# Performance work log

Measured on AMD Instinct MI355X. Metric: run time of the kernel, lower is better.

## Reference

```python
import jax, jax.numpy as jnp
import numpy as np

N_KW, N_RT = 100000, 20000
D, H, O = 128, 128, 128
E_A, E_B, E_C = 1600000, 1600000, 320000


def setup_inputs() -> dict:
    key = jax.random.key(0)
    ks = jax.random.split(key, 32)
    inp = {
        "x_kw": jax.random.normal(ks[0], (N_KW, D), jnp.float32),
        "x_rt": jax.random.normal(ks[1], (N_RT, D), jnp.float32),
        "src_a": jax.random.randint(ks[2], (E_A,), 0, N_RT),
        "dst_a": jax.random.randint(ks[3], (E_A,), 0, N_KW),
        "src_b": jax.random.randint(ks[4], (E_B,), 0, N_KW),
        "dst_b": jax.random.randint(ks[5], (E_B,), 0, N_KW),
        "src_c": jax.random.randint(ks[6], (E_C,), 0, N_RT),
        "dst_c": jax.random.randint(ks[7], (E_C,), 0, N_RT),
    }
    # SAGEConv params per relation per layer: W_l (neighbor), b_l, W_r (root, no bias)
    i = 8
    dims = {1: (D, H), 2: (H, O)}
    for layer in (1, 2):
        din, dout = dims[layer]
        for rel in ("a", "b", "c"):
            inp[f"Wl{layer}{rel}"] = jax.random.normal(ks[i], (din, dout), jnp.float32) * 0.05; i += 1
            inp[f"bl{layer}{rel}"] = jnp.zeros((dout,), jnp.float32)
            inp[f"Wr{layer}{rel}"] = jax.random.normal(ks[i], (din, dout), jnp.float32) * 0.05; i += 1
    return inp


def _sage(x_src, x_dst, src, dst, Wl, bl, Wr):
    # PyG SAGEConv (mean aggr): lin_l(mean_j x_src[j]) + lin_r(x_dst)
    n = x_dst.shape[0]
    s = jax.ops.segment_sum(x_src[src], dst, num_segments=n)      # [n, din]
    cnt = jax.ops.segment_sum(jnp.ones_like(dst, dtype=x_src.dtype), dst, num_segments=n)
    mean = s / jnp.maximum(cnt, 1.0)[:, None]
    return mean @ Wl + bl + x_dst @ Wr


def reference(x_kw, x_rt, src_a, dst_a, src_b, dst_b, src_c, dst_c,
              Wl1a, bl1a, Wr1a, Wl1b, bl1b, Wr1b, Wl1c, bl1c, Wr1c,
              Wl2a, bl2a, Wr2a, Wl2b, bl2b, Wr2b, Wl2c, bl2c, Wr2c):
    # layer 1 (HeteroConv aggr='sum' over relations sharing a dst type)
    kw1 = (_sage(x_rt, x_kw, src_a, dst_a, Wl1a, bl1a, Wr1a)
           + _sage(x_kw, x_kw, src_b, dst_b, Wl1b, bl1b, Wr1b))
    rt1 = _sage(x_rt, x_rt, src_c, dst_c, Wl1c, bl1c, Wr1c)
    kw1 = jax.nn.relu(kw1)
    rt1 = jax.nn.relu(rt1)
    # layer 2
    kw2 = (_sage(rt1, kw1, src_a, dst_a, Wl2a, bl2a, Wr2a)
           + _sage(kw1, kw1, src_b, dst_b, Wl2b, bl2b, Wr2b))
    rt2 = _sage(rt1, rt1, src_c, dst_c, Wl2c, bl2c, Wr2c)
    return kw2, rt2
```

## Files before the change

kernel.cpp:

```cpp
#include <hip/hip_runtime.h>

typedef __attribute__((ext_vector_type(8))) short bf16x8;
typedef __attribute__((ext_vector_type(4))) float f32x4;
typedef __attribute__((ext_vector_type(2))) float f32x2;

static __device__ __forceinline__ unsigned short f2bf(float f) {
    unsigned int u = __float_as_uint(f);
    u += 0x7fffu + ((u >> 16) & 1u);
    return (unsigned short)(u >> 16);
}
static __device__ __forceinline__ float bf2f(unsigned short h) {
    return __uint_as_float(((unsigned int)h) << 16);
}

#define BSH 6
#define BUCKET 64
#define NBMAX 1600
#define CHSH 13


struct PrepArgs {
    const float* W[10];
    const float* Wa[10];
    const float* b1a; const float* b1b; const float* b2a; const float* b2b;
};

__global__ void prep_k(PrepArgs pa, unsigned short* __restrict__ Wt,
                       float* __restrict__ bc1, float* __restrict__ bc2) {
    int blk = blockIdx.x;
    if (blk < 640) {
        int slot = blk >> 6;
        int i = ((blk & 63) << 8) + threadIdx.x;
        float v = pa.W[slot][i];
        const float* w2 = pa.Wa[slot];
        if (w2) v += w2[i];
        int k = i >> 7, n = i & 127;
        Wt[slot * 16384 + n * 128 + k] = f2bf(v);
    } else {
        int t = threadIdx.x;
        if (t < 128) bc1[t] = pa.b1a[t] + pa.b1b[t];
        else bc2[t - 128] = pa.b2a[t - 128] + pa.b2b[t - 128];
    }
}


struct Rel {
    const int* src; const int* dst; int E; int nb; int Ndst;
    int hblk0, hnblk;
    int sblk0, snblk;
    int oblk0;
    int* bcnt; int* boff; int* bcur;
    unsigned* pairs; unsigned* ssrc; int* goff; float* invd;
};
struct Rels { Rel r[3]; };

__global__ void bhist3_k(Rels R) {
    const Rel* r;
    int bid = blockIdx.x;
    if (bid < R.r[1].hblk0) r = &R.r[0];
    else if (bid < R.r[2].hblk0) r = &R.r[1];
    else r = &R.r[2];
    __shared__ int h[NBMAX];
    for (int i = threadIdx.x; i < r->nb; i += 256) h[i] = 0;
    __syncthreads();
    for (int e = (bid - r->hblk0) * 256 + threadIdx.x; e < r->E; e += r->hnblk * 256)
        atomicAdd(&h[r->dst[e] >> BSH], 1);
    __syncthreads();
    for (int i = threadIdx.x; i < r->nb; i += 256)
        if (h[i]) atomicAdd(&r->bcnt[i], h[i]);
}

__global__ void bscan3_k(Rels R) {
    const Rel* r = &R.r[blockIdx.x];
    __shared__ int s[1024];
    int t = threadIdx.x;
    int nb = r->nb;
    int e0 = 2 * t, e1 = 2 * t + 1;
    int v0 = (e0 < nb) ? r->bcnt[e0] : 0;
    int v1 = (e1 < nb) ? r->bcnt[e1] : 0;
    s[t] = v0 + v1;
    __syncthreads();
    for (int o = 1; o < 1024; o <<= 1) {
        int x = (t >= o) ? s[t - o] : 0;
        __syncthreads();
        s[t] += x;
        __syncthreads();
    }
    int P = s[t] - (v0 + v1);
    if (e0 <= nb) { r->boff[e0] = P; if (e0 < nb) r->bcur[e0] = 0; }
    if (e1 <= nb) { r->boff[e1] = P + v0; if (e1 < nb) r->bcur[e1] = 0; }
}

__global__ __launch_bounds__(256) void bscatter3_k(Rels R) {
    const Rel* r;
    int bid = blockIdx.x;
    if (bid < R.r[1].sblk0) r = &R.r[0];
    else if (bid < R.r[2].sblk0) r = &R.r[1];
    else r = &R.r[2];
    __shared__ int h[NBMAX];
    __shared__ int base[NBMAX];
    int t = threadIdx.x;
    int nb = r->nb, E = r->E;
    for (int i = t; i < nb; i += 256) h[i] = 0;
    __syncthreads();
    int e0 = (bid - r->sblk0) * 8192;
    for (int i = 0; i < 32; i++) {
        int e = e0 + i * 256 + t;
        if (e < E) atomicAdd(&h[r->dst[e] >> BSH], 1);
    }
    __syncthreads();
    for (int i = t; i < nb; i += 256) {
        int c = h[i];
        base[i] = c ? (r->boff[i] + atomicAdd(&r->bcur[i], c)) : 0;
    }
    __syncthreads();
    for (int i = t; i < nb; i += 256) h[i] = 0;
    __syncthreads();
    for (int i = 0; i < 32; i++) {
        int e = e0 + i * 256 + t;
        if (e < E) {
            int d = r->dst[e];
            int b = d >> BSH;
            int pos = base[b] + atomicAdd(&h[b], 1);
            r->pairs[pos] = ((unsigned)(d & (BUCKET - 1)) << 17) | (unsigned)r->src[e];
        }
    }
}

__global__ __launch_bounds__(256) void sortb3_k(Rels R) {
    const Rel* r;
    int bid = blockIdx.x;
    if (bid < R.r[1].oblk0) r = &R.r[0];
    else if (bid < R.r[2].oblk0) r = &R.r[1];
    else r = &R.r[2];
    int b = bid - r->oblk0;
    __shared__ int cnt[1024];
    __shared__ int sc[256];
    int t = threadIdx.x;
    for (int i = t; i < 1024; i += 256) cnt[i] = 0;
    __syncthreads();
    int j0 = r->boff[b], j1 = r->boff[b + 1];
    for (int j = j0 + t; j < j1; j += 256) {
        unsigned p = r->pairs[j];
        int d = (p >> 17) & 63;
        int ch = (int)((p & 0x1ffffu) >> CHSH); if (ch > 15) ch = 15;
        int bin = ((d & 7) << 7) | ((d >> 3) << 4) | ch;
        atomicAdd(&cnt[bin], 1);
    }
    __syncthreads();
    if (t < 64) {
        int b0 = ((t & 7) << 7) | ((t >> 3) << 4);
        int c = 0;
#pragma unroll
        for (int i = 0; i < 16; i++) c += cnt[b0 + i];
        int dd = (b << BSH) + t;
        if (dd < r->Ndst) r->invd[dd] = 1.f / (float)(c > 0 ? c : 1);
    }
    int c0 = cnt[4 * t], c1 = cnt[4 * t + 1], c2 = cnt[4 * t + 2], c3 = cnt[4 * t + 3];
    int tot = c0 + c1 + c2 + c3;
    sc[t] = tot;
    __syncthreads();
    for (int o = 1; o < 256; o <<= 1) {
        int x = (t >= o) ? sc[t - o] : 0;
        __syncthreads();
        sc[t] += x;
        __syncthreads();
    }
    int base = j0 + sc[t] - tot;
    if ((t & 3) == 0) r->goff[b * 64 + (t >> 2)] = base;
    cnt[4 * t] = base;
    cnt[4 * t + 1] = base + c0;
    cnt[4 * t + 2] = base + c0 + c1;
    cnt[4 * t + 3] = base + c0 + c1 + c2;
    if (t == 0 && b == r->nb - 1) r->goff[r->nb * 64] = r->E;
    __syncthreads();
    for (int j = j0 + t; j < j1; j += 256) {
        unsigned p = r->pairs[j];
        int d = (p >> 17) & 63;
        int ch = (int)((p & 0x1ffffu) >> CHSH); if (ch > 15) ch = 15;
        int bin = ((d & 7) << 7) | ((d >> 3) << 4) | ch;
        int pos = atomicAdd(&cnt[bin], 1);
        r->ssrc[pos] = p & 0x1ffffu;
    }
}


struct GemmJobs {
    const void* Akw; int Nkw;
    const unsigned short* Wk1; const float* bk; unsigned short* Zkw;
    const unsigned short* Wk2; unsigned short* Ckw;
    const void* Art; int Nrt;
    const unsigned short* Wr1; const float* br; unsigned short* Zrt;
    const unsigned short* Wr2; unsigned short* Crt2;
    const unsigned short* Wr3; unsigned short* Crt3;
    int kwBlocks;
};

template <int AF32>
__global__ __launch_bounds__(256) void gemm3_k(GemmJobs G) {
    int bid = blockIdx.x;
    bool iskw = bid < G.kwBlocks;
    const void* A = iskw ? G.Akw : G.Art;
    int N = iskw ? G.Nkw : G.Nrt;
    int lane = threadIdx.x & 63;
    int r16 = lane & 15, g = lane >> 4;
    int row0 = (iskw ? bid : bid - G.kwBlocks) * 64 + (threadIdx.x >> 6) * 16;
    int arow = row0 + r16;
    int arow_c = arow < N ? arow : N - 1;

    bf16x8 af[4];
    if (AF32) {
        const float* Af = (const float*)A + (size_t)arow_c * 128 + g * 8;
#pragma unroll
        for (int kc = 0; kc < 4; kc++) {
            float4 u0 = *(const float4*)(Af + kc * 32);
            float4 u1 = *(const float4*)(Af + kc * 32 + 4);
            bf16x8 r;
            r[0] = (short)f2bf(u0.x); r[1] = (short)f2bf(u0.y);
            r[2] = (short)f2bf(u0.z); r[3] = (short)f2bf(u0.w);
            r[4] = (short)f2bf(u1.x); r[5] = (short)f2bf(u1.y);
            r[6] = (short)f2bf(u1.z); r[7] = (short)f2bf(u1.w);
            af[kc] = r;
        }
    } else {
        const bf16x8* Ar = (const bf16x8*)((const unsigned short*)A + (size_t)arow_c * 128);
#pragma unroll
        for (int kc = 0; kc < 4; kc++) af[kc] = Ar[kc * 4 + g];
    }

    if (iskw) {
        f32x4 acc1[8], acc2[8];
#pragma unroll
        for (int ct = 0; ct < 8; ct++) { f32x4 z = {0.f,0.f,0.f,0.f}; acc1[ct] = z; acc2[ct] = z; }
#pragma unroll
        for (int kc = 0; kc < 4; kc++) {
#pragma unroll
            for (int ct = 0; ct < 8; ct++) {
                int wo = ((ct * 16 + r16) << 7) + kc * 32 + g * 8;
                bf16x8 b1 = *(const bf16x8*)(G.Wk1 + wo);
                acc1[ct] = __builtin_amdgcn_mfma_f32_16x16x32_bf16(af[kc], b1, acc1[ct], 0, 0, 0);
                bf16x8 b2 = *(const bf16x8*)(G.Wk2 + wo);
                acc2[ct] = __builtin_amdgcn_mfma_f32_16x16x32_bf16(af[kc], b2, acc2[ct], 0, 0, 0);
            }
        }
#pragma unroll
        for (int ct = 0; ct < 8; ct++) {
            int col = ct * 16 + r16;
            float bb = G.bk[col];
#pragma unroll
            for (int j = 0; j < 4; j++) {
                int r = row0 + g * 4 + j;
                if (r < N) {
                    G.Zkw[(size_t)r * 128 + col] = f2bf(acc1[ct][j] + bb);
                    G.Ckw[(size_t)r * 128 + col] = f2bf(acc2[ct][j]);
                }
            }
        }
    } else {
        f32x4 acc1[8], acc2[8], acc3[8];
#pragma unroll
        for (int ct = 0; ct < 8; ct++) {
            f32x4 z = {0.f,0.f,0.f,0.f}; acc1[ct] = z; acc2[ct] = z; acc3[ct] = z;
        }
#pragma unroll
        for (int kc = 0; kc < 4; kc++) {
#pragma unroll
            for (int ct = 0; ct < 8; ct++) {
                int wo = ((ct * 16 + r16) << 7) + kc * 32 + g * 8;
                bf16x8 b1 = *(const bf16x8*)(G.Wr1 + wo);
                acc1[ct] = __builtin_amdgcn_mfma_f32_16x16x32_bf16(af[kc], b1, acc1[ct], 0, 0, 0);
                bf16x8 b2 = *(const bf16x8*)(G.Wr2 + wo);
                acc2[ct] = __builtin_amdgcn_mfma_f32_16x16x32_bf16(af[kc], b2, acc2[ct], 0, 0, 0);
                bf16x8 b3 = *(const bf16x8*)(G.Wr3 + wo);
                acc3[ct] = __builtin_amdgcn_mfma_f32_16x16x32_bf16(af[kc], b3, acc3[ct], 0, 0, 0);
            }
        }
#pragma unroll
        for (int ct = 0; ct < 8; ct++) {
            int col = ct * 16 + r16;
            float bb = G.br[col];
#pragma unroll
            for (int j = 0; j < 4; j++) {
                int r = row0 + g * 4 + j;
                if (r < N) {
                    G.Zrt[(size_t)r * 128 + col] = f2bf(acc1[ct][j] + bb);
                    G.Crt2[(size_t)r * 128 + col] = f2bf(acc2[ct][j]);
                    G.Crt3[(size_t)r * 128 + col] = f2bf(acc3[ct][j]);
                }
            }
        }
    }
}

struct AggJob {
    const unsigned short* Zin; int Ndst;
    const unsigned* sp0; const int* goff0; const float* invd0; const unsigned short* Y0;
    const unsigned* sp1; const int* goff1; const float* invd1; const unsigned short* Y1;
    int nrel;
    float* OutF; unsigned short* OutB;
};

template <int RELU, int OUTBF16>
__global__ __launch_bounds__(512) void bagg2_k(AggJob JK, AggJob JR, int kwBlocks) {
    __shared__ float acc[BUCKET * 128];
    bool iskw = blockIdx.x < kwBlocks;
    AggJob J = iskw ? JK : JR;
    int b = iskw ? blockIdx.x : blockIdx.x - kwBlocks;
    int t = threadIdx.x;
    int dst0 = b << BSH;
    int nrow = J.Ndst - dst0; if (nrow > BUCKET) nrow = BUCKET;

    for (int c = t; c < BUCKET * 32; c += 512) {
        int r = c >> 5, m = c & 31;
        float z0 = 0.f, z1 = 0.f, z2 = 0.f, z3 = 0.f;
        if (r < nrow) {
            ushort4 z = *(const ushort4*)(J.Zin + (size_t)(dst0 + r) * 128 + (m << 2));
            z0 = bf2f(z.x); z1 = bf2f(z.y); z2 = bf2f(z.z); z3 = bf2f(z.w);
        }
        acc[r * 128 + m] = z0;
        acc[r * 128 + 32 + m] = z1;
        acc[r * 128 + 64 + m] = z2;
        acc[r * 128 + 96 + m] = z3;
    }
    __syncthreads();

    int w = t >> 6, lane = t & 63;
    int h = lane >> 5, q = lane & 31;
#pragma unroll 1
    for (int rel = 0; rel < J.nrel; rel++) {
        const unsigned* sp = rel ? J.sp1 : J.sp0;
        const int* goff = rel ? J.goff1 : J.goff0;
        const float* invd = rel ? J.invd1 : J.invd0;
        const unsigned short* Y = rel ? J.Y1 : J.Y0;
#pragma unroll 1
        for (int r = 0; r < 8; r++) {
            int g = b * 64 + w * 8 + r;
            int jg0 = goff[g], jg1 = goff[g + 1];
            if (jg0 >= jg1) continue;
            int d = (r << 3) | w;
            f32x2 a01 = {0.f, 0.f}, a23 = {0.f, 0.f};
#pragma unroll 1
            for (int j = jg0; j < jg1; j += 16) {
                uint2 v[8];
#pragma unroll
                for (int k = 0; k < 8; k++) {
                    int e = j + 2 * k + h;
                    e = e < jg1 ? e : jg1 - 1;
                    int s = (int)sp[e];
                    v[k] = *(const uint2*)(Y + ((size_t)s << 7) + (q << 2));
                }
#pragma unroll
                for (int k = 0; k < 8; k++) {
                    bool ok = (j + 2 * k + h) < jg1;
                    unsigned vx = ok ? v[k].x : 0u;
                    unsigned vy = ok ? v[k].y : 0u;
                    f32x2 x01 = { __uint_as_float(vx << 16),
                                  __uint_as_float(vx & 0xffff0000u) };
                    f32x2 x23 = { __uint_as_float(vy << 16),
                                  __uint_as_float(vy & 0xffff0000u) };
                    a01 += x01;
                    a23 += x23;
                }
            }
            a01.x += __shfl_xor(a01.x, 32); a01.y += __shfl_xor(a01.y, 32);
            a23.x += __shfl_xor(a23.x, 32); a23.y += __shfl_xor(a23.y, 32);
            float inv = invd[dst0 + d];
            float v0 = (h ? a23.x : a01.x) * inv;
            float v1 = (h ? a23.y : a01.y) * inv;
            int ba = d * 128 + q + h * 64;
            acc[ba] += v0;
            acc[ba + 32] += v1;
        }
    }
    __syncthreads();
    for (int c = t; c < BUCKET * 32; c += 512) {
        int r = c >> 5, m = c & 31;
        if (r < nrow) {
            float x0 = acc[r * 128 + m];
            float x1 = acc[r * 128 + 32 + m];
            float x2 = acc[r * 128 + 64 + m];
            float x3 = acc[r * 128 + 96 + m];
            if (RELU) {
                x0 = fmaxf(x0, 0.f); x1 = fmaxf(x1, 0.f);
                x2 = fmaxf(x2, 0.f); x3 = fmaxf(x3, 0.f);
            }
            size_t o = (size_t)(dst0 + r) * 128 + (m << 2);
            if (OUTBF16) {
                ushort4 ov;
                ov.x = f2bf(x0); ov.y = f2bf(x1); ov.z = f2bf(x2); ov.w = f2bf(x3);
                *(ushort4*)(J.OutB + o) = ov;
            } else {
                *(float4*)(J.OutF + o) = make_float4(x0, x1, x2, x3);
            }
        }
    }
}


static inline size_t align256(size_t x) { return (x + 255) & ~size_t(255); }

extern "C" void kernel_launch(void* const* d_in, const int* in_sizes, int n_in,
                              void* d_out, int out_size, void* d_ws, size_t ws_size,
                              hipStream_t stream) {
    const float* x_kw = (const float*)d_in[0];
    const float* x_rt = (const float*)d_in[1];
    const int* src_a = (const int*)d_in[2];
    const int* dst_a = (const int*)d_in[3];
    const int* src_b = (const int*)d_in[4];
    const int* dst_b = (const int*)d_in[5];
    const int* src_c = (const int*)d_in[6];
    const int* dst_c = (const int*)d_in[7];
    const float *Wl1a = (const float*)d_in[8],  *bl1a = (const float*)d_in[9],  *Wr1a = (const float*)d_in[10];
    const float *Wl1b = (const float*)d_in[11], *bl1b = (const float*)d_in[12], *Wr1b = (const float*)d_in[13];
    const float *Wl1c = (const float*)d_in[14], *bl1c = (const float*)d_in[15], *Wr1c = (const float*)d_in[16];
    const float *Wl2a = (const float*)d_in[17], *bl2a = (const float*)d_in[18], *Wr2a = (const float*)d_in[19];
    const float *Wl2b = (const float*)d_in[20], *bl2b = (const float*)d_in[21], *Wr2b = (const float*)d_in[22];
    const float *Wl2c = (const float*)d_in[23], *bl2c = (const float*)d_in[24], *Wr2c = (const float*)d_in[25];

    const int NKW = in_sizes[0] / 128;
    const int NRT = in_sizes[1] / 128;
    const int EA = in_sizes[2], EB = in_sizes[4], EC = in_sizes[6];
    const int nb_kw = (NKW + BUCKET - 1) / BUCKET;
    const int nb_rt = (NRT + BUCKET - 1) / BUCKET;

    char* ws = (char*)d_ws;
    size_t off = 0;
    auto alloc = [&](size_t bytes) -> char* {
        off = align256(off);
        char* p = ws + off;
        off += bytes;
        return p;
    };
    unsigned short* Wt = (unsigned short*)alloc(10 * 16384 * 2);
    float* bc1 = (float*)alloc(128 * 4);
    float* bc2 = (float*)alloc(128 * 4);
    int* bcnt3 = (int*)alloc(3 * NBMAX * 4);
    int* bcur3 = (int*)alloc(3 * NBMAX * 4);
    int* boff_a = (int*)alloc((NBMAX + 1) * 4);
    int* boff_b = (int*)alloc((NBMAX + 1) * 4);
    int* boff_c = (int*)alloc((NBMAX + 1) * 4);
    int* goff_a = (int*)alloc(((size_t)nb_kw * 64 + 1) * 4);
    int* goff_b = (int*)alloc(((size_t)nb_kw * 64 + 1) * 4);
    int* goff_c = (int*)alloc(((size_t)nb_rt * 64 + 1) * 4);
    float* invd_a = (float*)alloc((size_t)NKW * 4);
    float* invd_b = (float*)alloc((size_t)NKW * 4);
    float* invd_c = (float*)alloc((size_t)NRT * 4);
    unsigned* pairs_a = (unsigned*)alloc((size_t)EA * 4);
    unsigned* pairs_b = (unsigned*)alloc((size_t)EB * 4);
    unsigned* pairs_c = (unsigned*)alloc((size_t)EC * 4);
    unsigned* sp_a = (unsigned*)alloc((size_t)EA * 4);
    unsigned* sp_b = (unsigned*)alloc((size_t)EB * 4);
    unsigned* sp_c = (unsigned*)alloc((size_t)EC * 4);
    unsigned short* Yb = (unsigned short*)alloc((size_t)NKW * 128 * 2);
    unsigned short* Zkw = (unsigned short*)alloc((size_t)NKW * 128 * 2);
    unsigned short* Zrt = (unsigned short*)alloc((size_t)NRT * 128 * 2);
    unsigned short* kw1_bf = (unsigned short*)alloc((size_t)NKW * 128 * 2);
    unsigned short* rt1_bf = (unsigned short*)alloc((size_t)NRT * 128 * 2);
    (void)ws_size;
    unsigned short* Ya = (unsigned short*)pairs_b;
    unsigned short* Yc = (unsigned short*)pairs_a;

    float* out_kw = (float*)d_out;
    float* out_rt = out_kw + (size_t)NKW * 128;

    PrepArgs pa;
    pa.W[0] = Wr1a; pa.Wa[0] = Wr1b;
    pa.W[1] = Wl1a; pa.Wa[1] = nullptr;
    pa.W[2] = Wl1b; pa.Wa[2] = nullptr;
    pa.W[3] = Wl1c; pa.Wa[3] = nullptr;
    pa.W[4] = Wr1c; pa.Wa[4] = nullptr;
    pa.W[5] = Wr2a; pa.Wa[5] = Wr2b;
    pa.W[6] = Wl2a; pa.Wa[6] = nullptr;
    pa.W[7] = Wl2b; pa.Wa[7] = nullptr;
    pa.W[8] = Wl2c; pa.Wa[8] = nullptr;
    pa.W[9] = Wr2c; pa.Wa[9] = nullptr;
    pa.b1a = bl1a; pa.b1b = bl1b; pa.b2a = bl2a; pa.b2b = bl2b;
    prep_k<<<641, 256, 0, stream>>>(pa, Wt, bc1, bc2);
    unsigned short* W0 = Wt + 0 * 16384;
    unsigned short* W1 = Wt + 1 * 16384;
    unsigned short* W2 = Wt + 2 * 16384;
    unsigned short* W3 = Wt + 3 * 16384;
    unsigned short* W4 = Wt + 4 * 16384;
    unsigned short* W5 = Wt + 5 * 16384;
    unsigned short* W6 = Wt + 6 * 16384;
    unsigned short* W7 = Wt + 7 * 16384;
    unsigned short* W8 = Wt + 8 * 16384;
    unsigned short* W9 = Wt + 9 * 16384;

    hipMemsetAsync(bcnt3, 0, 3 * NBMAX * 4, stream);
    Rels R;
    int hA = 128, hB = 128, hC = 64;
    int sA = (EA + 8191) / 8192, sB = (EB + 8191) / 8192, sC = (EC + 8191) / 8192;
    R.r[0] = {src_a, dst_a, EA, nb_kw, NKW, 0, hA, 0, sA, 0,
              bcnt3, boff_a, bcur3, pairs_a, sp_a, goff_a, invd_a};
    R.r[1] = {src_b, dst_b, EB, nb_kw, NKW, hA, hB, sA, sB, nb_kw,
              bcnt3 + NBMAX, boff_b, bcur3 + NBMAX, pairs_b, sp_b, goff_b, invd_b};
    R.r[2] = {src_c, dst_c, EC, nb_rt, NRT, hA + hB, hC, sA + sB, sC, 2 * nb_kw,
              bcnt3 + 2 * NBMAX, boff_c, bcur3 + 2 * NBMAX, pairs_c, sp_c, goff_c, invd_c};
    bhist3_k<<<hA + hB + hC, 256, 0, stream>>>(R);
    bscan3_k<<<3, 1024, 0, stream>>>(R);
    bscatter3_k<<<sA + sB + sC, 256, 0, stream>>>(R);
    sortb3_k<<<2 * nb_kw + nb_rt, 256, 0, stream>>>(R);

    const int kwB = (NKW + 63) / 64, rtB = (NRT + 63) / 64;

    GemmJobs G1;
    G1.Akw = x_kw; G1.Nkw = NKW; G1.Wk1 = W0; G1.bk = bc1; G1.Zkw = Zkw; G1.Wk2 = W2; G1.Ckw = Yb;
    G1.Art = x_rt; G1.Nrt = NRT; G1.Wr1 = W4; G1.br = bl1c; G1.Zrt = Zrt;
    G1.Wr2 = W1; G1.Crt2 = Ya; G1.Wr3 = W3; G1.Crt3 = Yc;
    G1.kwBlocks = kwB;
    gemm3_k<1><<<kwB + rtB, 256, 0, stream>>>(G1);

    AggJob JK1 = {Zkw, NKW, sp_a, goff_a, invd_a, Ya, sp_b, goff_b, invd_b, Yb, 2,
                  nullptr, kw1_bf};
    AggJob JR1 = {Zrt, NRT, sp_c, goff_c, invd_c, Yc, nullptr, nullptr, nullptr, nullptr, 1,
                  nullptr, rt1_bf};
    bagg2_k<1, 1><<<nb_kw + nb_rt, 512, 0, stream>>>(JK1, JR1, nb_kw);

    GemmJobs G2;
    G2.Akw = kw1_bf; G2.Nkw = NKW; G2.Wk1 = W5; G2.bk = bc2; G2.Zkw = Zkw; G2.Wk2 = W7; G2.Ckw = Yb;
    G2.Art = rt1_bf; G2.Nrt = NRT; G2.Wr1 = W9; G2.br = bl2c; G2.Zrt = Zrt;
    G2.Wr2 = W6; G2.Crt2 = Ya; G2.Wr3 = W8; G2.Crt3 = Yc;
    G2.kwBlocks = kwB;
    gemm3_k<0><<<kwB + rtB, 256, 0, stream>>>(G2);

    AggJob JK2 = {Zkw, NKW, sp_a, goff_a, invd_a, Ya, sp_b, goff_b, invd_b, Yb, 2,
                  out_kw, nullptr};
    AggJob JR2 = {Zrt, NRT, sp_c, goff_c, invd_c, Yc, nullptr, nullptr, nullptr, nullptr, 1,
                  out_rt, nullptr};
    bagg2_k<0, 0><<<nb_kw + nb_rt, 512, 0, stream>>>(JK2, JR2, nb_kw);
}
```

Before: 580.3 us.

## Store relation-b messages in FP8, pre-shift gather offsets, fuse prep/hist and gemm/sort kernels

The relation-b projected features (kw->kw, the largest edge set) are now written as FP8 instead of BF16, which halves the bytes gathered per edge in aggregation. Sorted source indices are pre-shifted into byte offsets so the gather loop does no index arithmetic. The weight prep kernel is merged with the histogram kernel, and the sort kernel with the layer-1 GEMM, to cut launches and let independent work overlap. The aggregation loop is split into a full-chunk path and a masked tail. The cost is lower precision for one relation's messages, with added accuracy risk, plus separate Ya/Yc buffers instead of reusing the pairs buffers.

New measurement: 595.8 us. 1.03x slower.

```diff
diff --git a/kernel.cpp b/kernel.cpp
--- a/kernel.cpp
+++ b/kernel.cpp
@@ -18,6 +18,17 @@
 #define NBMAX 1600
 #define CHSH 13
 
+
+struct Rel {
+    const int* src; const int* dst; int E; int nb; int Ndst;
+    int hblk0, hnblk;
+    int sblk0, snblk;
+    int oblk0;
+    int shift;
+    int* bcnt; int* boff; int* bcur;
+    unsigned* pairs; unsigned* ssrc; int* goff; float* invd;
+};
+struct Rels { Rel r[3]; };
 
 struct PrepArgs {
     const float* W[10];
@@ -25,50 +36,42 @@
     const float* b1a; const float* b1b; const float* b2a; const float* b2b;
 };
 
-__global__ void prep_k(PrepArgs pa, unsigned short* __restrict__ Wt,
-                       float* __restrict__ bc1, float* __restrict__ bc2) {
-    int blk = blockIdx.x;
-    if (blk < 640) {
-        int slot = blk >> 6;
-        int i = ((blk & 63) << 8) + threadIdx.x;
-        float v = pa.W[slot][i];
-        const float* w2 = pa.Wa[slot];
-        if (w2) v += w2[i];
-        int k = i >> 7, n = i & 127;
-        Wt[slot * 16384 + n * 128 + k] = f2bf(v);
-    } else {
-        int t = threadIdx.x;
-        if (t < 128) bc1[t] = pa.b1a[t] + pa.b1b[t];
-        else bc2[t - 128] = pa.b2a[t - 128] + pa.b2b[t - 128];
-    }
-}
-
-
-struct Rel {
-    const int* src; const int* dst; int E; int nb; int Ndst;
-    int hblk0, hnblk;
-    int sblk0, snblk;
-    int oblk0;
-    int* bcnt; int* boff; int* bcur;
-    unsigned* pairs; unsigned* ssrc; int* goff; float* invd;
-};
-struct Rels { Rel r[3]; };
-
-__global__ void bhist3_k(Rels R) {
+
+__global__ void prep_hist_k(PrepArgs pa, unsigned short* __restrict__ Wt,
+                            float* __restrict__ bc1, float* __restrict__ bc2,
+                            Rels R, int prepBlocks) {
+    int bid = blockIdx.x;
+    if (bid < prepBlocks) {
+        if (bid < 640) {
+            int slot = bid >> 6;
+            int i = ((bid & 63) << 8) + threadIdx.x;
+            float v = pa.W[slot][i];
+            const float* w2 = pa.Wa[slot];
+            if (w2) v += w2[i];
+            int k = i >> 7, n = i & 127;
+            Wt[slot * 16384 + n * 128 + k] = f2bf(v);
+        } else {
+            int t = threadIdx.x;
+            if (t < 128) bc1[t] = pa.b1a[t] + pa.b1b[t];
+            else bc2[t - 128] = pa.b2a[t - 128] + pa.b2b[t - 128];
+        }
+        return;
+    }
+    int hb = bid - prepBlocks;
     const Rel* r;
-    int bid = blockIdx.x;
-    if (bid < R.r[1].hblk0) r = &R.r[0];
-    else if (bid < R.r[2].hblk0) r = &R.r[1];
+    if (hb < R.r[1].hblk0) r = &R.r[0];
+    else if (hb < R.r[2].hblk0) r = &R.r[1];
     else r = &R.r[2];
     __shared__ int h[NBMAX];
     for (int i = threadIdx.x; i < r->nb; i += 256) h[i] = 0;
     __syncthreads();
-    for (int e = (bid - r->hblk0) * 256 + threadIdx.x; e < r->E; e += r->hnblk * 256)
+    for (int e = (hb - r->hblk0) * 256 + threadIdx.x; e < r->E; e += r->hnblk * 256)
         atomicAdd(&h[r->dst[e] >> BSH], 1);
     __syncthreads();
     for (int i = threadIdx.x; i < r->nb; i += 256)
         if (h[i]) atomicAdd(&r->bcnt[i], h[i]);
 }
+
 
 __global__ void bscan3_k(Rels R) {
     const Rel* r = &R.r[blockIdx.x];
@@ -127,9 +130,8 @@
     }
 }
 
-__global__ __launch_bounds__(256) void sortb3_k(Rels R) {
+static __device__ void sortb_body(const Rels& R, int bid) {
     const Rel* r;
-    int bid = blockIdx.x;
     if (bid < R.r[1].oblk0) r = &R.r[0];
     else if (bid < R.r[2].oblk0) r = &R.r[1];
     else r = &R.r[2];
@@ -174,13 +176,14 @@
     cnt[4 * t + 3] = base + c0 + c1 + c2;
     if (t == 0 && b == r->nb - 1) r->goff[r->nb * 64] = r->E;
     __syncthreads();
+    int shift = r->shift;
     for (int j = j0 + t; j < j1; j += 256) {
         unsigned p = r->pairs[j];
         int d = (p >> 17) & 63;
         int ch = (int)((p & 0x1ffffu) >> CHSH); if (ch > 15) ch = 15;
         int bin = ((d & 7) << 7) | ((d >> 3) << 4) | ch;
         int pos = atomicAdd(&cnt[bin], 1);
-        r->ssrc[pos] = p & 0x1ffffu;
+        r->ssrc[pos] = (p & 0x1ffffu) << shift;
     }
 }
 
@@ -188,7 +191,7 @@
 struct GemmJobs {
     const void* Akw; int Nkw;
     const unsigned short* Wk1; const float* bk; unsigned short* Zkw;
-    const unsigned short* Wk2; unsigned short* Ckw;
+    const unsigned short* Wk2; unsigned char* Ckw8;
     const void* Art; int Nrt;
     const unsigned short* Wr1; const float* br; unsigned short* Zrt;
     const unsigned short* Wr2; unsigned short* Crt2;
@@ -197,8 +200,7 @@
 };
 
 template <int AF32>
-__global__ __launch_bounds__(256) void gemm3_k(GemmJobs G) {
-    int bid = blockIdx.x;
+static __device__ void gemm_body(const GemmJobs& G, int bid) {
     bool iskw = bid < G.kwBlocks;
     const void* A = iskw ? G.Akw : G.Art;
     int N = iskw ? G.Nkw : G.Nrt;
@@ -215,12 +217,12 @@
         for (int kc = 0; kc < 4; kc++) {
             float4 u0 = *(const float4*)(Af + kc * 32);
             float4 u1 = *(const float4*)(Af + kc * 32 + 4);
-            bf16x8 r;
-            r[0] = (short)f2bf(u0.x); r[1] = (short)f2bf(u0.y);
-            r[2] = (short)f2bf(u0.z); r[3] = (short)f2bf(u0.w);
-            r[4] = (short)f2bf(u1.x); r[5] = (short)f2bf(u1.y);
-            r[6] = (short)f2bf(u1.z); r[7] = (short)f2bf(u1.w);
-            af[kc] = r;
+            bf16x8 rr;
+            rr[0] = (short)f2bf(u0.x); rr[1] = (short)f2bf(u0.y);
+            rr[2] = (short)f2bf(u0.z); rr[3] = (short)f2bf(u0.w);
+            rr[4] = (short)f2bf(u1.x); rr[5] = (short)f2bf(u1.y);
+            rr[6] = (short)f2bf(u1.z); rr[7] = (short)f2bf(u1.w);
+            af[kc] = rr;
         }
     } else {
         const bf16x8* Ar = (const bf16x8*)((const unsigned short*)A + (size_t)arow_c * 128);
@@ -252,7 +254,9 @@
                 int r = row0 + g * 4 + j;
                 if (r < N) {
                     G.Zkw[(size_t)r * 128 + col] = f2bf(acc1[ct][j] + bb);
-                    G.Ckw[(size_t)r * 128 + col] = f2bf(acc2[ct][j]);
+                    float v2 = acc2[ct][j];
+                    int pk = __builtin_amdgcn_cvt_pk_fp8_f32(v2, v2, 0, false);
+                    G.Ckw8[(size_t)r * 128 + col] = (unsigned char)(pk & 0xff);
                 }
             }
         }
@@ -292,10 +296,122 @@
     }
 }
 
+__global__ __launch_bounds__(256) void gemm_sort_k(GemmJobs G, Rels R, int gemmBlocks) {
+    if ((int)blockIdx.x < gemmBlocks) gemm_body<1>(G, blockIdx.x);
+    else sortb_body(R, blockIdx.x - gemmBlocks);
+}
+
+__global__ __launch_bounds__(256) void gemm_l2_k(GemmJobs G) {
+    gemm_body<0>(G, blockIdx.x);
+}
+
+template <int FMT>
+static __device__ __forceinline__ void agg_rel(float* acc, int b, int w, int h, int q,
+                                               int dst0,
+                                               const unsigned* __restrict__ sp,
+                                               const int* __restrict__ goff,
+                                               const float* __restrict__ invd,
+                                               const char* __restrict__ Ybase) {
+    int lanebyte = FMT ? (q << 2) : (q << 3);
+#pragma unroll 1
+    for (int r = 0; r < 8; r++) {
+        int g = b * 64 + w * 8 + r;
+        int jg0 = goff[g], jg1 = goff[g + 1];
+        if (jg0 >= jg1) continue;
+        int d = (r << 3) | w;
+        f32x2 a01 = {0.f, 0.f}, a23 = {0.f, 0.f};
+        int len = jg1 - jg0;
+        int j = jg0;
+        int jfull = jg0 + (len & ~15);
+#pragma unroll 1
+        for (; j < jfull; j += 16) {
+            unsigned off[8];
+#pragma unroll
+            for (int k = 0; k < 8; k++) off[k] = sp[j + 2 * k + h];
+            if (FMT == 0) {
+                uint2 v[8];
+#pragma unroll
+                for (int k = 0; k < 8; k++)
+                    v[k] = *(const uint2*)(Ybase + off[k] + lanebyte);
+#pragma unroll
+                for (int k = 0; k < 8; k++) {
+                    f32x2 x01 = { __uint_as_float(v[k].x << 16),
+                                  __uint_as_float(v[k].x & 0xffff0000u) };
+                    f32x2 x23 = { __uint_as_float(v[k].y << 16),
+                                  __uint_as_float(v[k].y & 0xffff0000u) };
+                    a01 += x01;
+                    a23 += x23;
+                }
+            } else {
+                unsigned v[8];
+#pragma unroll
+                for (int k = 0; k < 8; k++)
+                    v[k] = *(const unsigned*)(Ybase + off[k] + lanebyte);
+#pragma unroll
+                for (int k = 0; k < 8; k++) {
+                    auto lo = __builtin_amdgcn_cvt_pk_f32_fp8(v[k], false);
+                    auto hi = __builtin_amdgcn_cvt_pk_f32_fp8(v[k], true);
+                    a01[0] += lo[0]; a01[1] += lo[1];
+                    a23[0] += hi[0]; a23[1] += hi[1];
+                }
+            }
+        }
+        if (j < jg1) {
+            if (FMT == 0) {
+                uint2 v[8];
+#pragma unroll
+                for (int k = 0; k < 8; k++) {
+                    int e = j + 2 * k + h;
+                    int ec = e < jg1 ? e : jg1 - 1;
+                    uint2 t2 = *(const uint2*)(Ybase + sp[ec] + lanebyte);
+                    bool ok = e < jg1;
+                    v[k].x = ok ? t2.x : 0u;
+                    v[k].y = ok ? t2.y : 0u;
+                }
+#pragma unroll
+                for (int k = 0; k < 8; k++) {
+                    f32x2 x01 = { __uint_as_float(v[k].x << 16),
+                                  __uint_as_float(v[k].x & 0xffff0000u) };
+                    f32x2 x23 = { __uint_as_float(v[k].y << 16),
+                                  __uint_as_float(v[k].y & 0xffff0000u) };
+                    a01 += x01;
+                    a23 += x23;
+                }
+            } else {
+                unsigned v[8];
+#pragma unroll
+                for (int k = 0; k < 8; k++) {
+                    int e = j + 2 * k + h;
+                    int ec = e < jg1 ? e : jg1 - 1;
+                    unsigned tv = *(const unsigned*)(Ybase + sp[ec] + lanebyte);
+                    v[k] = (e < jg1) ? tv : 0u;
+                }
+#pragma unroll
+                for (int k = 0; k < 8; k++) {
+                    auto lo = __builtin_amdgcn_cvt_pk_f32_fp8(v[k], false);
+                    auto hi = __builtin_amdgcn_cvt_pk_f32_fp8(v[k], true);
+                    a01[0] += lo[0]; a01[1] += lo[1];
+                    a23[0] += hi[0]; a23[1] += hi[1];
+                }
+            }
+        }
+        a01[0] += __shfl_xor(a01[0], 32);
+        a01[1] += __shfl_xor(a01[1], 32);
+        a23[0] += __shfl_xor(a23[0], 32);
+        a23[1] += __shfl_xor(a23[1], 32);
+        float inv = invd[dst0 + d];
+        float v0 = (h ? a23[0] : a01[0]) * inv;
+        float v1 = (h ? a23[1] : a01[1]) * inv;
+        int ba = d * 128 + q + h * 64;
+        acc[ba] += v0;
+        acc[ba + 32] += v1;
+    }
+}
+
 struct AggJob {
     const unsigned short* Zin; int Ndst;
-    const unsigned* sp0; const int* goff0; const float* invd0; const unsigned short* Y0;
-    const unsigned* sp1; const int* goff1; const float* invd1; const unsigned short* Y1;
+    const unsigned* sp0; const int* goff0; const float* invd0; const void* Y0; int fmt0;
+    const unsigned* sp1; const int* goff1; const float* invd1; const void* Y1; int fmt1;
     int nrel;
     float* OutF; unsigned short* OutB;
 };
@@ -303,7 +419,7 @@
 template <int RELU, int OUTBF16>
 __global__ __launch_bounds__(512) void bagg2_k(AggJob JK, AggJob JR, int kwBlocks) {
     __shared__ float acc[BUCKET * 128];
-    bool iskw = blockIdx.x < kwBlocks;
+    bool iskw = blockIdx.x < (unsigned)kwBlocks;
     AggJob J = iskw ? JK : JR;
     int b = iskw ? blockIdx.x : blockIdx.x - kwBlocks;
     int t = threadIdx.x;
@@ -326,51 +442,11 @@
 
     int w = t >> 6, lane = t & 63;
     int h = lane >> 5, q = lane & 31;
-#pragma unroll 1
-    for (int rel = 0; rel < J.nrel; rel++) {
-        const unsigned* sp = rel ? J.sp1 : J.sp0;
-        const int* goff = rel ? J.goff1 : J.goff0;
-        const float* invd = rel ? J.invd1 : J.invd0;
-        const unsigned short* Y = rel ? J.Y1 : J.Y0;
-#pragma unroll 1
-        for (int r = 0; r < 8; r++) {
-            int g = b * 64 + w * 8 + r;
-            int jg0 = goff[g], jg1 = goff[g + 1];
-            if (jg0 >= jg1) continue;
-            int d = (r << 3) | w;
-            f32x2 a01 = {0.f, 0.f}, a23 = {0.f, 0.f};
-#pragma unroll 1
-            for (int j = jg0; j < jg1; j += 16) {
-                uint2 v[8];
-#pragma unroll
-                for (int k = 0; k < 8; k++) {
-                    int e = j + 2 * k + h;
-                    e = e < jg1 ? e : jg1 - 1;
-                    int s = (int)sp[e];
-                    v[k] = *(const uint2*)(Y + ((size_t)s << 7) + (q << 2));
-                }
-#pragma unroll
-                for (int k = 0; k < 8; k++) {
-                    bool ok = (j + 2 * k + h) < jg1;
-                    unsigned vx = ok ? v[k].x : 0u;
-                    unsigned vy = ok ? v[k].y : 0u;
-                    f32x2 x01 = { __uint_as_float(vx << 16),
-                                  __uint_as_float(vx & 0xffff0000u) };
-                    f32x2 x23 = { __uint_as_float(vy << 16),
-                                  __uint_as_float(vy & 0xffff0000u) };
-                    a01 += x01;
-                    a23 += x23;
-                }
-            }
-            a01.x += __shfl_xor(a01.x, 32); a01.y += __shfl_xor(a01.y, 32);
-            a23.x += __shfl_xor(a23.x, 32); a23.y += __shfl_xor(a23.y, 32);
-            float inv = invd[dst0 + d];
-            float v0 = (h ? a23.x : a01.x) * inv;
-            float v1 = (h ? a23.y : a01.y) * inv;
-            int ba = d * 128 + q + h * 64;
-            acc[ba] += v0;
-            acc[ba + 32] += v1;
-        }
+    if (J.fmt0 == 0) agg_rel<0>(acc, b, w, h, q, dst0, J.sp0, J.goff0, J.invd0, (const char*)J.Y0);
+    else agg_rel<1>(acc, b, w, h, q, dst0, J.sp0, J.goff0, J.invd0, (const char*)J.Y0);
+    if (J.nrel == 2) {
+        if (J.fmt1 == 0) agg_rel<0>(acc, b, w, h, q, dst0, J.sp1, J.goff1, J.invd1, (const char*)J.Y1);
+        else agg_rel<1>(acc, b, w, h, q, dst0, J.sp1, J.goff1, J.invd1, (const char*)J.Y1);
     }
     __syncthreads();
     for (int c = t; c < BUCKET * 32; c += 512) {
@@ -451,18 +527,29 @@
     unsigned* sp_a = (unsigned*)alloc((size_t)EA * 4);
     unsigned* sp_b = (unsigned*)alloc((size_t)EB * 4);
     unsigned* sp_c = (unsigned*)alloc((size_t)EC * 4);
-    unsigned short* Yb = (unsigned short*)alloc((size_t)NKW * 128 * 2);
+    unsigned short* Ya = (unsigned short*)alloc((size_t)NRT * 128 * 2);
+    unsigned char*  Yb = (unsigned char*)alloc((size_t)NKW * 128);
+    unsigned short* Yc = (unsigned short*)alloc((size_t)NRT * 128 * 2);
     unsigned short* Zkw = (unsigned short*)alloc((size_t)NKW * 128 * 2);
     unsigned short* Zrt = (unsigned short*)alloc((size_t)NRT * 128 * 2);
     unsigned short* kw1_bf = (unsigned short*)alloc((size_t)NKW * 128 * 2);
     unsigned short* rt1_bf = (unsigned short*)alloc((size_t)NRT * 128 * 2);
     (void)ws_size;
-    unsigned short* Ya = (unsigned short*)pairs_b;
-    unsigned short* Yc = (unsigned short*)pairs_a;
 
     float* out_kw = (float*)d_out;
     float* out_rt = out_kw + (size_t)NKW * 128;
 
+    Rels R;
+    int hA = 128, hB = 128, hC = 64;
+    int sA = (EA + 8191) / 8192, sB = (EB + 8191) / 8192, sC = (EC + 8191) / 8192;
+    R.r[0] = {src_a, dst_a, EA, nb_kw, NKW, 0, hA, 0, sA, 0, 8,
+              bcnt3, boff_a, bcur3, pairs_a, sp_a, goff_a, invd_a};
+    R.r[1] = {src_b, dst_b, EB, nb_kw, NKW, hA, hB, sA, sB, nb_kw, 7,
+              bcnt3 + NBMAX, boff_b, bcur3 + NBMAX, pairs_b, sp_b, goff_b, invd_b};
+    R.r[2] = {src_c, dst_c, EC, nb_rt, NRT, hA + hB, hC, sA + sB, sC, 2 * nb_kw, 8,
+              bcnt3 + 2 * NBMAX, boff_c, bcur3 + 2 * NBMAX, pairs_c, sp_c, goff_c, invd_c};
+
+    hipMemsetAsync(bcnt3, 0, 3 * NBMAX * 4, stream);
     PrepArgs pa;
     pa.W[0] = Wr1a; pa.Wa[0] = Wr1b;
     pa.W[1] = Wl1a; pa.Wa[1] = nullptr;
@@ -475,7 +562,7 @@
     pa.W[8] = Wl2c; pa.Wa[8] = nullptr;
     pa.W[9] = Wr2c; pa.Wa[9] = nullptr;
     pa.b1a = bl1a; pa.b1b = bl1b; pa.b2a = bl2a; pa.b2b = bl2b;
-    prep_k<<<641, 256, 0, stream>>>(pa, Wt, bc1, bc2);
+    prep_hist_k<<<641 + hA + hB + hC, 256, 0, stream>>>(pa, Wt, bc1, bc2, R, 641);
     unsigned short* W0 = Wt + 0 * 16384;
     unsigned short* W1 = Wt + 1 * 16384;
     unsigned short* W2 = Wt + 2 * 16384;
@@ -487,46 +574,35 @@
     unsigned short* W8 = Wt + 8 * 16384;
     unsigned short* W9 = Wt + 9 * 16384;
 
-    hipMemsetAsync(bcnt3, 0, 3 * NBMAX * 4, stream);
-    Rels R;
-    int hA = 128, hB = 128, hC = 64;
-    int sA = (EA + 8191) / 8192, sB = (EB + 8191) / 8192, sC = (EC + 8191) / 8192;
-    R.r[0] = {src_a, dst_a, EA, nb_kw, NKW, 0, hA, 0, sA, 0,
-              bcnt3, boff_a, bcur3, pairs_a, sp_a, goff_a, invd_a};
-    R.r[1] = {src_b, dst_b, EB, nb_kw, NKW, hA, hB, sA, sB, nb_kw,
-              bcnt3 + NBMAX, boff_b, bcur3 + NBMAX, pairs_b, sp_b, goff_b, invd_b};
-    R.r[2] = {src_c, dst_c, EC, nb_rt, NRT, hA + hB, hC, sA + sB, sC, 2 * nb_kw,
-              bcnt3 + 2 * NBMAX, boff_c, bcur3 + 2 * NBMAX, pairs_c, sp_c, goff_c, invd_c};
-    bhist3_k<<<hA + hB + hC, 256, 0, stream>>>(R);
     bscan3_k<<<3, 1024, 0, stream>>>(R);
     bscatter3_k<<<sA + sB + sC, 256, 0, stream>>>(R);
-    sortb3_k<<<2 * nb_kw + nb_rt, 256, 0, stream>>>(R);
 
     const int kwB = (NKW + 63) / 64, rtB = (NRT + 63) / 64;
+    const int nsort = 2 * nb_kw + nb_rt;
 
     GemmJobs G1;
-    G1.Akw = x_kw; G1.Nkw = NKW; G1.Wk1 = W0; G1.bk = bc1; G1.Zkw = Zkw; G1.Wk2 = W2; G1.Ckw = Yb;
+    G1.Akw = x_kw; G1.Nkw = NKW; G1.Wk1 = W0; G1.bk = bc1; G1.Zkw = Zkw; G1.Wk2 = W2; G1.Ckw8 = Yb;
     G1.Art = x_rt; G1.Nrt = NRT; G1.Wr1 = W4; G1.br = bl1c; G1.Zrt = Zrt;
     G1.Wr2 = W1; G1.Crt2 = Ya; G1.Wr3 = W3; G1.Crt3 = Yc;
     G1.kwBlocks = kwB;
-    gemm3_k<1><<<kwB + rtB, 256, 0, stream>>>(G1);
-
-    AggJob JK1 = {Zkw, NKW, sp_a, goff_a, invd_a, Ya, sp_b, goff_b, invd_b, Yb, 2,
+    gemm_sort_k<<<kwB + rtB + nsort, 256, 0, stream>>>(G1, R, kwB + rtB);
+
+    AggJob JK1 = {Zkw, NKW, sp_a, goff_a, invd_a, Ya, 0, sp_b, goff_b, invd_b, Yb, 1, 2,
                   nullptr, kw1_bf};
-    AggJob JR1 = {Zrt, NRT, sp_c, goff_c, invd_c, Yc, nullptr, nullptr, nullptr, nullptr, 1,
+    AggJob JR1 = {Zrt, NRT, sp_c, goff_c, invd_c, Yc, 0, nullptr, nullptr, nullptr, nullptr, 0, 1,
                   nullptr, rt1_bf};
     bagg2_k<1, 1><<<nb_kw + nb_rt, 512, 0, stream>>>(JK1, JR1, nb_kw);
 
     GemmJobs G2;
-    G2.Akw = kw1_bf; G2.Nkw = NKW; G2.Wk1 = W5; G2.bk = bc2; G2.Zkw = Zkw; G2.Wk2 = W7; G2.Ckw = Yb;
+    G2.Akw = kw1_bf; G2.Nkw = NKW; G2.Wk1 = W5; G2.bk = bc2; G2.Zkw = Zkw; G2.Wk2 = W7; G2.Ckw8 = Yb;
     G2.Art = rt1_bf; G2.Nrt = NRT; G2.Wr1 = W9; G2.br = bl2c; G2.Zrt = Zrt;
     G2.Wr2 = W6; G2.Crt2 = Ya; G2.Wr3 = W8; G2.Crt3 = Yc;
     G2.kwBlocks = kwB;
-    gemm3_k<0><<<kwB + rtB, 256, 0, stream>>>(G2);
-
-    AggJob JK2 = {Zkw, NKW, sp_a, goff_a, invd_a, Ya, sp_b, goff_b, invd_b, Yb, 2,
+    gemm_l2_k<<<kwB + rtB, 256, 0, stream>>>(G2);
+
+    AggJob JK2 = {Zkw, NKW, sp_a, goff_a, invd_a, Ya, 0, sp_b, goff_b, invd_b, Yb, 1, 2,
                   out_kw, nullptr};
-    AggJob JR2 = {Zrt, NRT, sp_c, goff_c, invd_c, Yc, nullptr, nullptr, nullptr, nullptr, 1,
+    AggJob JR2 = {Zrt, NRT, sp_c, goff_c, invd_c, Yc, 0, nullptr, nullptr, nullptr, nullptr, 0, 1,
                   out_rt, nullptr};
     bagg2_k<0, 0><<<nb_kw + nb_rt, 512, 0, stream>>>(JK2, JR2, nb_kw);
 }
```
